# Optimization experiments

Measured on AMD Instinct MI355X. Metric: run time of the kernel, lower is better.

The kernel has to match this reference:

```python
import jax, jax.numpy as jnp
import numpy as np

D = 8192          # dimension (high_dim_mode since > 1000)
M = 1_600_000     # ~0.05 * D*(D-1) pairs after the i>j mask
RIEMANN_SHIFT = 0.5


def _lower_tri_pairs(rng, d, m):
    # Sample m unique strictly-lower-triangular (i, j) positions (i > j).
    total = d * (d - 1) // 2
    k = rng.choice(total, size=m, replace=False)
    kf = k.astype(np.float64)
    i = np.floor((1.0 + np.sqrt(1.0 + 8.0 * kf)) / 2.0).astype(np.int64)
    # fix possible off-by-one from float sqrt
    tri = i * (i - 1) // 2
    i = np.where(tri > k, i - 1, i)
    tri = i * (i - 1) // 2
    j = k - tri
    return i, j


def setup_inputs() -> dict:
    key = jax.random.key(0)
    k1, k2 = jax.random.split(key)
    rng = np.random.default_rng(0)

    i, j = _lower_tri_pairs(rng, D, M)
    interaction_indices = jnp.asarray(np.stack([i, j]))  # [2, M] int64

    local_scale = 1.0 / D ** 0.75
    h_local = jax.random.normal(k1, (D,), dtype=jnp.float32) * local_scale + RIEMANN_SHIFT

    dim_factor = 1.0 / (D ** 0.9 * np.log(D))
    V_interaction = jax.random.normal(k2, (M,), dtype=jnp.float32) * dim_factor

    return {
        "h_local": h_local,
        "V_interaction": V_interaction,
        "interaction_indices": interaction_indices,
        "dimension": D,
    }


def reference(h_local, V_interaction, interaction_indices, dimension) -> jnp.ndarray:
    d = h_local.shape[0]
    # scatter interaction values into strict lower triangle (set semantics,
    # indices are unique so set == torch assignment)
    H_int = jnp.zeros((d, d), dtype=h_local.dtype)
    H_int = H_int.at[interaction_indices[0], interaction_indices[1]].set(V_interaction)
    H_int = H_int + H_int.T  # symmetrize
    interaction_scale = 1.0 - 0.2 / np.sqrt(np.log(dimension))
    return jnp.diag(h_local) + H_int * interaction_scale
```

## Files before the change

kernel.cpp:

```cpp
#include <hip/hip_runtime.h>
#include <math.h>


#define P1_PAIRS 4096
#define NBKT     2048
#define BCAP     8
#define OVB      512
#define SENTK    0xFFFFFFFFu
#define GCAP     65536


__global__ __launch_bounds__(64) void zero_hdr_kernel(int* __restrict__ ghdr)
{
    if (threadIdx.x == 0) ghdr[0] = 0;
}

__global__ __launch_bounds__(1024) void p1_kernel(
    const int*   __restrict__ idx,
    const float* __restrict__ vals,
    float scale, int m, int nblk,
    uint2* __restrict__ region1,
    uint2* __restrict__ ovf,
    int*   __restrict__ ovfc,
    uint2* __restrict__ glist,
    int*   __restrict__ ghdr)
{
    __shared__ uint2 stage[NBKT][BCAP];
    __shared__ int   cnt[NBKT];
    __shared__ uint2 ovfst[OVB];
    __shared__ int   ovfn;

    uint2* sflat = &stage[0][0];
    for (int f = threadIdx.x; f < NBKT * BCAP; f += 1024)
        sflat[f] = make_uint2(SENTK, 0u);
    for (int b = threadIdx.x; b < NBKT; b += 1024) cnt[b] = 0;
    if (threadIdx.x == 0) ovfn = 0;
    __syncthreads();

    const int blk  = blockIdx.x;
    const int base = blk * P1_PAIRS;
#pragma unroll
    for (int it = 0; it < P1_PAIRS / 1024; ++it) {
        int k = base + it * 1024 + threadIdx.x;
        if (k < m) {
            int i = idx[k];
            int j = idx[m + k];
            unsigned vb = __float_as_uint(vals[k] * scale);

            unsigned k1 = ((unsigned)i << 13) | (unsigned)j;
            int b1 = i >> 2;
            int p = atomicAdd(&cnt[b1], 1);
            if (p < BCAP) stage[b1][p] = make_uint2(k1, vb);
            else {
                int q = atomicAdd(&ovfn, 1);
                if (q < OVB) ovfst[q] = make_uint2(k1, vb);
                else { int g = atomicAdd(ghdr, 1); if (g < GCAP) glist[g] = make_uint2(k1, vb); }
            }

            unsigned k2 = ((unsigned)j << 13) | (unsigned)i;
            int b2 = j >> 2;
            p = atomicAdd(&cnt[b2], 1);
            if (p < BCAP) stage[b2][p] = make_uint2(k2, vb);
            else {
                int q = atomicAdd(&ovfn, 1);
                if (q < OVB) ovfst[q] = make_uint2(k2, vb);
                else { int g = atomicAdd(ghdr, 1); if (g < GCAP) glist[g] = make_uint2(k2, vb); }
            }
        }
    }
    __syncthreads();

    for (int f = threadIdx.x; f < NBKT * BCAP; f += 1024) {
        int b = f >> 3, e = f & 7;
        region1[((long long)b * nblk + blk) * BCAP + e] = sflat[f];
    }
    int n = ovfn; if (n > OVB) n = OVB;
    for (int e = threadIdx.x; e < n; e += 1024)
        ovf[(long long)blk * OVB + e] = ovfst[e];
    if (threadIdx.x == 0) ovfc[blk] = n;
}

__global__ __launch_bounds__(1024) void p2_kernel(
    float* __restrict__ out,
    const float* __restrict__ h_local,
    const uint2* __restrict__ region1,
    int nblk)
{
    __shared__ float srow[4 * 8192];
    float4* s4 = reinterpret_cast<float4*>(srow);
    const int band = blockIdx.x;

    for (int c = threadIdx.x; c < 8192; c += 1024)
        s4[c] = make_float4(0.f, 0.f, 0.f, 0.f);
    __syncthreads();

    const uint4* src = reinterpret_cast<const uint4*>(
        region1 + (long long)band * nblk * BCAP);
    const int n2 = (nblk * BCAP) >> 1;
    for (int e = threadIdx.x; e < n2; e += 1024) {
        uint4 en = src[e];
        if (en.x != SENTK) srow[en.x & 0x7FFF] = __uint_as_float(en.y);
        if (en.z != SENTK) srow[en.z & 0x7FFF] = __uint_as_float(en.w);
    }
    if (threadIdx.x < 4) {
        int r = (band << 2) + threadIdx.x;
        srow[((unsigned)threadIdx.x << 13) | (unsigned)r] = h_local[r];
    }
    __syncthreads();

    float4* orow = reinterpret_cast<float4*>(out + ((long long)band << 15));
    for (int c = threadIdx.x; c < 8192; c += 1024)
        orow[c] = s4[c];
}

__global__ __launch_bounds__(256) void ovf_scatter_kernel(
    float* __restrict__ out,
    const uint2* __restrict__ ovf,
    const int*   __restrict__ ovfc,
    const uint2* __restrict__ glist,
    const int*   __restrict__ ghdr)
{
    const int blk = blockIdx.x;
    int n = ovfc[blk]; if (n > OVB) n = OVB;
    for (int e = threadIdx.x; e < n; e += 256) {
        uint2 en = ovf[(long long)blk * OVB + e];
        out[en.x] = __uint_as_float(en.y);
    }
    if (blk == 0) {
        int g = ghdr[0]; if (g > GCAP) g = GCAP;
        for (int e = threadIdx.x; e < g; e += 256) {
            uint2 en = glist[e];
            out[en.x] = __uint_as_float(en.y);
        }
    }
}


__global__ __launch_bounds__(256) void init_counts_kernel(
    float* __restrict__ out, int d, int logd)
{
    int r = blockIdx.x * blockDim.x + threadIdx.x;
    if (r < d) reinterpret_cast<int*>(out)[(long long)r << logd] = 0;
}

__global__ __launch_bounds__(256) void bin_kernel(
    float* __restrict__ out,
    const int*   __restrict__ idx,
    const float* __restrict__ vals,
    float scale, int m, int logd, int cap)
{
    int k = blockIdx.x * blockDim.x + threadIdx.x;
    if (k >= m) return;
    int i = idx[k];
    int j = idx[m + k];
    unsigned vb = __float_as_uint(vals[k] * scale);
    int* cnt_i = reinterpret_cast<int*>(out) + ((long long)i << logd);
    int* cnt_j = reinterpret_cast<int*>(out) + ((long long)j << logd);
    int p1 = atomicAdd(cnt_i, 1);
    if (p1 < cap)
        *reinterpret_cast<uint2*>(out + ((long long)i << logd) + 2 + 2 * p1) =
            make_uint2((unsigned)j, vb);
    int p2 = atomicAdd(cnt_j, 1);
    if (p2 < cap)
        *reinterpret_cast<uint2*>(out + ((long long)j << logd) + 2 + 2 * p2) =
            make_uint2((unsigned)i, vb);
}

__global__ __launch_bounds__(256) void rows_kernel(
    float* __restrict__ out,
    const float* __restrict__ h_local,
    int logd, int cap)
{
    __shared__ float srow[8192];
    const int d  = 1 << logd;
    const int n4 = d >> 2;
    float4* s4 = reinterpret_cast<float4*>(srow);
    const int r = blockIdx.x;
    float* grow = out + ((long long)r << logd);
    const float4 z = make_float4(0.f, 0.f, 0.f, 0.f);
    for (int c = threadIdx.x; c < n4; c += blockDim.x) s4[c] = z;
    __syncthreads();
    int cnt = reinterpret_cast<const int*>(grow)[0];
    if (cnt > cap) cnt = cap;
    const uint2* eb = reinterpret_cast<const uint2*>(grow + 2);
    for (int e = threadIdx.x; e < cnt; e += blockDim.x) {
        uint2 p = eb[e];
        srow[p.x] = __uint_as_float(p.y);
    }
    if (threadIdx.x == 0) srow[r] = h_local[r];
    __syncthreads();
    for (int c = threadIdx.x; c < n4; c += blockDim.x)
        reinterpret_cast<float4*>(grow)[c] = s4[c];
}

__global__ __launch_bounds__(256) void fill_diag_kernel(
    float* __restrict__ out, const float* __restrict__ h_local,
    int d, long long n)
{
    long long t = (long long)blockIdx.x * blockDim.x + threadIdx.x;
    if (t >= n) return;
    long long row = t / d;
    long long col = t - row * d;
    out[t] = (row == col) ? h_local[row] : 0.f;
}

__global__ __launch_bounds__(256) void scatter_kernel(
    float* __restrict__ out,
    const int* __restrict__ idx,
    const float* __restrict__ vals,
    float scale, int m, int d)
{
    int k = blockIdx.x * blockDim.x + threadIdx.x;
    if (k >= m) return;
    int i = idx[k];
    int j = idx[m + k];
    float v = vals[k] * scale;
    out[(long long)i * d + j] = v;
    out[(long long)j * d + i] = v;
}


extern "C" void kernel_launch(void* const* d_in, const int* in_sizes, int n_in,
                              void* d_out, int out_size, void* d_ws, size_t ws_size,
                              hipStream_t stream) {
    const float* h_local = (const float*)d_in[0];
    const float* V_int   = (const float*)d_in[1];
    const int*   idx     = (const int*)d_in[2];

    const int d = in_sizes[0];
    const int m = in_sizes[1];

    int logd = 0;
    while ((1 << logd) < d) ++logd;
    const bool pow2 = ((1 << logd) == d);

    const float iscale = (float)(1.0 - 0.2 / sqrt(log((double)d)));
    float* out = (float*)d_out;
    const int block = 256;

    const int nblk = (m + P1_PAIRS - 1) / P1_PAIRS;

    const size_t off_ovfc  = 4096;
    const size_t off_glist = off_ovfc + (((size_t)nblk * 4 + 4095) & ~(size_t)4095);
    const size_t off_ovf   = off_glist + (size_t)GCAP * sizeof(uint2);
    const size_t off_r1    = off_ovf + (((size_t)nblk * OVB * sizeof(uint2) + 4095)
                                        & ~(size_t)4095);
    const size_t ws_need   = off_r1 + (size_t)NBKT * nblk * BCAP * sizeof(uint2);

    const bool path6 = (d == 8192) && (m > 0) && (m <= 2000000) &&
                       (d_ws != nullptr) && (ws_size >= ws_need);

    if (path6) {
        char* ws = (char*)d_ws;
        int*   ghdr    = (int*)ws;
        int*   ovfc    = (int*)(ws + off_ovfc);
        uint2* glist   = (uint2*)(ws + off_glist);
        uint2* ovf     = (uint2*)(ws + off_ovf);
        uint2* region1 = (uint2*)(ws + off_r1);

        zero_hdr_kernel<<<1, 64, 0, stream>>>(ghdr);
        p1_kernel<<<nblk, 1024, 0, stream>>>(idx, V_int, iscale, m, nblk,
                                             region1, ovf, ovfc, glist, ghdr);
        p2_kernel<<<NBKT, 1024, 0, stream>>>(out, h_local, region1, nblk);
        ovf_scatter_kernel<<<nblk, 256, 0, stream>>>(out, ovf, ovfc, glist, ghdr);
    } else if (pow2 && d >= 1024 && d <= 8192 &&
               ((long long)m * 2 / d) < (long long)((d - 2) / 2) / 2) {
        const int cap = (d - 2) / 2;
        init_counts_kernel<<<(d + block - 1) / block, block, 0, stream>>>(out, d, logd);
        bin_kernel<<<(m + block - 1) / block, block, 0, stream>>>(out, idx, V_int,
                                                                  iscale, m, logd, cap);
        rows_kernel<<<d, block, 0, stream>>>(out, h_local, logd, cap);
    } else {
        const long long n = (long long)d * d;
        const long long grid_fill = (n + block - 1) / block;
        fill_diag_kernel<<<(dim3)(unsigned)grid_fill, block, 0, stream>>>(out, h_local, d, n);
        const int grid_sc = (m + block - 1) / block;
        scatter_kernel<<<grid_sc, block, 0, stream>>>(out, idx, V_int, iscale, m, d);
    }
}
```

Before: 320.4 us.

## Fold overflow scatter into row-band kernel using per-band overflow buckets

Overflow entries from the binning pass now go into per-2-row-band global buckets via atomics, replacing the per-block list. The band kernel applies them in shared memory before writing rows, so the separate overflow scatter kernel and its random global writes disappear. The band kernel now handles 2 rows per block with 512 threads instead of 4 rows with 1024, and the header zeroing kernel becomes a memset. In exchange, each region1 band is read twice with a filter on the band bits, and the global list is scanned by every block if it is non-empty.

```diff
diff --git a/kernel.cpp b/kernel.cpp
--- a/kernel.cpp
+++ b/kernel.cpp
@@ -5,23 +5,20 @@
 #define P1_PAIRS 4096
 #define NBKT     2048
 #define BCAP     8
+#define NB2      4096
 #define OVB      512
+#define OVCAP    64
 #define SENTK    0xFFFFFFFFu
 #define GCAP     65536
 
-
-__global__ __launch_bounds__(64) void zero_hdr_kernel(int* __restrict__ ghdr)
-{
-    if (threadIdx.x == 0) ghdr[0] = 0;
-}
 
 __global__ __launch_bounds__(1024) void p1_kernel(
     const int*   __restrict__ idx,
     const float* __restrict__ vals,
     float scale, int m, int nblk,
     uint2* __restrict__ region1,
-    uint2* __restrict__ ovf,
-    int*   __restrict__ ovfc,
+    uint2* __restrict__ ovfreg,
+    int*   __restrict__ ovfcur,
     uint2* __restrict__ glist,
     int*   __restrict__ ghdr)
 {
@@ -51,21 +48,17 @@
             int b1 = i >> 2;
             int p = atomicAdd(&cnt[b1], 1);
             if (p < BCAP) stage[b1][p] = make_uint2(k1, vb);
-            else {
-                int q = atomicAdd(&ovfn, 1);
-                if (q < OVB) ovfst[q] = make_uint2(k1, vb);
-                else { int g = atomicAdd(ghdr, 1); if (g < GCAP) glist[g] = make_uint2(k1, vb); }
-            }
+            else { int q = atomicAdd(&ovfn, 1);
+                   if (q < OVB) ovfst[q] = make_uint2(k1, vb);
+                   else { int g = atomicAdd(ghdr, 1); if (g < GCAP) glist[g] = make_uint2(k1, vb); } }
 
             unsigned k2 = ((unsigned)j << 13) | (unsigned)i;
             int b2 = j >> 2;
             p = atomicAdd(&cnt[b2], 1);
             if (p < BCAP) stage[b2][p] = make_uint2(k2, vb);
-            else {
-                int q = atomicAdd(&ovfn, 1);
-                if (q < OVB) ovfst[q] = make_uint2(k2, vb);
-                else { int g = atomicAdd(ghdr, 1); if (g < GCAP) glist[g] = make_uint2(k2, vb); }
-            }
+            else { int q = atomicAdd(&ovfn, 1);
+                   if (q < OVB) ovfst[q] = make_uint2(k2, vb);
+                   else { int g = atomicAdd(ghdr, 1); if (g < GCAP) glist[g] = make_uint2(k2, vb); } }
         }
     }
     __syncthreads();
@@ -75,64 +68,64 @@
         region1[((long long)b * nblk + blk) * BCAP + e] = sflat[f];
     }
     int n = ovfn; if (n > OVB) n = OVB;
-    for (int e = threadIdx.x; e < n; e += 1024)
-        ovf[(long long)blk * OVB + e] = ovfst[e];
-    if (threadIdx.x == 0) ovfc[blk] = n;
-}
-
-__global__ __launch_bounds__(1024) void p2_kernel(
+    for (int e = threadIdx.x; e < n; e += 1024) {
+        uint2 en = ovfst[e];
+        int band2 = en.x >> 14;
+        int pos = atomicAdd(&ovfcur[band2], 1);
+        if (pos < OVCAP) ovfreg[band2 * OVCAP + pos] = en;
+        else { int g = atomicAdd(ghdr, 1); if (g < GCAP) glist[g] = en; }
+    }
+}
+
+__global__ __launch_bounds__(512) void p2_kernel(
     float* __restrict__ out,
     const float* __restrict__ h_local,
     const uint2* __restrict__ region1,
-    int nblk)
-{
-    __shared__ float srow[4 * 8192];
-    float4* s4 = reinterpret_cast<float4*>(srow);
-    const int band = blockIdx.x;
-
-    for (int c = threadIdx.x; c < 8192; c += 1024)
-        s4[c] = make_float4(0.f, 0.f, 0.f, 0.f);
-    __syncthreads();
-
-    const uint4* src = reinterpret_cast<const uint4*>(
-        region1 + (long long)band * nblk * BCAP);
-    const int n2 = (nblk * BCAP) >> 1;
-    for (int e = threadIdx.x; e < n2; e += 1024) {
-        uint4 en = src[e];
-        if (en.x != SENTK) srow[en.x & 0x7FFF] = __uint_as_float(en.y);
-        if (en.z != SENTK) srow[en.z & 0x7FFF] = __uint_as_float(en.w);
-    }
-    if (threadIdx.x < 4) {
-        int r = (band << 2) + threadIdx.x;
-        srow[((unsigned)threadIdx.x << 13) | (unsigned)r] = h_local[r];
-    }
-    __syncthreads();
-
-    float4* orow = reinterpret_cast<float4*>(out + ((long long)band << 15));
-    for (int c = threadIdx.x; c < 8192; c += 1024)
-        orow[c] = s4[c];
-}
-
-__global__ __launch_bounds__(256) void ovf_scatter_kernel(
-    float* __restrict__ out,
-    const uint2* __restrict__ ovf,
-    const int*   __restrict__ ovfc,
+    int nblk,
+    const uint2* __restrict__ ovfreg,
+    const int*   __restrict__ ovfcur,
     const uint2* __restrict__ glist,
     const int*   __restrict__ ghdr)
 {
-    const int blk = blockIdx.x;
-    int n = ovfc[blk]; if (n > OVB) n = OVB;
-    for (int e = threadIdx.x; e < n; e += 256) {
-        uint2 en = ovf[(long long)blk * OVB + e];
-        out[en.x] = __uint_as_float(en.y);
-    }
-    if (blk == 0) {
-        int g = ghdr[0]; if (g > GCAP) g = GCAP;
-        for (int e = threadIdx.x; e < g; e += 256) {
+    __shared__ float srow[2 * 8192];
+    float4* s4 = reinterpret_cast<float4*>(srow);
+    const int band2 = blockIdx.x;
+
+    for (int c = threadIdx.x; c < 4096; c += 512)
+        s4[c] = make_float4(0.f, 0.f, 0.f, 0.f);
+    __syncthreads();
+
+    const uint4* src = reinterpret_cast<const uint4*>(
+        region1 + (long long)(band2 >> 1) * nblk * BCAP);
+    const int n2 = (nblk * BCAP) >> 1;
+    const unsigned bu = (unsigned)band2;
+    for (int e = threadIdx.x; e < n2; e += 512) {
+        uint4 en = src[e];
+        if ((en.x >> 14) == bu) srow[en.x & 16383] = __uint_as_float(en.y);
+        if ((en.z >> 14) == bu) srow[en.z & 16383] = __uint_as_float(en.w);
+    }
+    int n = ovfcur[band2]; if (n > OVCAP) n = OVCAP;
+    for (int e = threadIdx.x; e < n; e += 512) {
+        uint2 en = ovfreg[band2 * OVCAP + e];
+        srow[en.x & 16383] = __uint_as_float(en.y);
+    }
+    int gn = ghdr[0];
+    if (gn > 0) {
+        if (gn > GCAP) gn = GCAP;
+        for (int e = threadIdx.x; e < gn; e += 512) {
             uint2 en = glist[e];
-            out[en.x] = __uint_as_float(en.y);
+            if ((en.x >> 14) == bu) srow[en.x & 16383] = __uint_as_float(en.y);
         }
     }
+    if (threadIdx.x < 2) {
+        int r = (band2 << 1) + threadIdx.x;
+        srow[((unsigned)threadIdx.x << 13) | (unsigned)r] = h_local[r];
+    }
+    __syncthreads();
+
+    float4* orow = reinterpret_cast<float4*>(out + ((long long)band2 << 14));
+    for (int c = threadIdx.x; c < 4096; c += 512)
+        orow[c] = s4[c];
 }
 
 
@@ -240,29 +233,29 @@
 
     const int nblk = (m + P1_PAIRS - 1) / P1_PAIRS;
 
-    const size_t off_ovfc  = 4096;
-    const size_t off_glist = off_ovfc + (((size_t)nblk * 4 + 4095) & ~(size_t)4095);
-    const size_t off_ovf   = off_glist + (size_t)GCAP * sizeof(uint2);
-    const size_t off_r1    = off_ovf + (((size_t)nblk * OVB * sizeof(uint2) + 4095)
-                                        & ~(size_t)4095);
-    const size_t ws_need   = off_r1 + (size_t)NBKT * nblk * BCAP * sizeof(uint2);
-
-    const bool path6 = (d == 8192) && (m > 0) && (m <= 2000000) &&
+    const size_t off_ovfcur = 4096;
+    const size_t hdr_bytes  = off_ovfcur + (size_t)NB2 * 4;
+    const size_t off_glist  = 24576;
+    const size_t off_ovfreg = off_glist + (size_t)GCAP * sizeof(uint2);
+    const size_t off_r1     = off_ovfreg + (size_t)NB2 * OVCAP * sizeof(uint2);
+    const size_t ws_need    = off_r1 + (size_t)NBKT * nblk * BCAP * sizeof(uint2);
+
+    const bool path7 = (d == 8192) && (m > 0) && (m <= 2000000) &&
                        (d_ws != nullptr) && (ws_size >= ws_need);
 
-    if (path6) {
+    if (path7) {
         char* ws = (char*)d_ws;
         int*   ghdr    = (int*)ws;
-        int*   ovfc    = (int*)(ws + off_ovfc);
+        int*   ovfcur  = (int*)(ws + off_ovfcur);
         uint2* glist   = (uint2*)(ws + off_glist);
-        uint2* ovf     = (uint2*)(ws + off_ovf);
+        uint2* ovfreg  = (uint2*)(ws + off_ovfreg);
         uint2* region1 = (uint2*)(ws + off_r1);
 
-        zero_hdr_kernel<<<1, 64, 0, stream>>>(ghdr);
+        hipMemsetAsync(ws, 0, hdr_bytes, stream);
         p1_kernel<<<nblk, 1024, 0, stream>>>(idx, V_int, iscale, m, nblk,
-                                             region1, ovf, ovfc, glist, ghdr);
-        p2_kernel<<<NBKT, 1024, 0, stream>>>(out, h_local, region1, nblk);
-        ovf_scatter_kernel<<<nblk, 256, 0, stream>>>(out, ovf, ovfc, glist, ghdr);
+                                             region1, ovfreg, ovfcur, glist, ghdr);
+        p2_kernel<<<NB2, 512, 0, stream>>>(out, h_local, region1, nblk,
+                                           ovfreg, ovfcur, glist, ghdr);
     } else if (pow2 && d >= 1024 && d <= 8192 &&
                ((long long)m * 2 / d) < (long long)((d - 2) / 2) / 2) {
         const int cap = (d - 2) / 2;
```

Result: slower. 328.2 us (+2.5%).
